# Kernel tuning notes

Hardware: AMD Instinct MI355X
Metric: run time of the kernel (lower is better)

The kernel has to match this reference:

```python
import jax, jax.numpy as jnp
import numpy as np

T, E, H, V, K = 1024, 300, 512, 100000, 12
START, STOP = 10, 11


def setup_inputs() -> dict:
    key = jax.random.key(0)
    ks = jax.random.split(key, 12)
    s = 0.05
    sentence = jax.random.randint(ks[0], (T,), 0, V, dtype=jnp.int32)
    tags = jax.random.randint(ks[1], (T,), 0, START, dtype=jnp.int32)  # real tags only
    word_embeds = jax.random.normal(ks[2], (V, E), jnp.float32) * 0.1

    def lstm_p(k):
        k1, k2 = jax.random.split(k)
        return (jax.random.normal(k1, (4 * H, E), jnp.float32) * s,
                jax.random.normal(k2, (4 * H, H), jnp.float32) * s,
                jnp.zeros(4 * H, jnp.float32), jnp.zeros(4 * H, jnp.float32))

    Wih_f, Whh_f, bih_f, bhh_f = lstm_p(ks[3])
    Wih_b, Whh_b, bih_b, bhh_b = lstm_p(ks[4])
    D = 2 * H
    attn_W = jax.random.normal(ks[5], (D, D), jnp.float32) * s
    attn_b = jnp.zeros(D, jnp.float32)
    h2h1_W = jax.random.normal(ks[6], (D, 2 * D), jnp.float32) * s
    h2h1_b = jnp.zeros(D, jnp.float32)
    tag_W = jax.random.normal(ks[7], (K, D), jnp.float32) * s
    tag_b = jnp.zeros(K, jnp.float32)
    transitions = jax.random.normal(ks[8], (K, K), jnp.float32) * 0.01
    transitions = transitions.at[START, :].set(-10000.0).at[:, STOP].set(-10000.0)
    return dict(sentence=sentence, tags=tags, word_embeds=word_embeds,
                Wih_f=Wih_f, Whh_f=Whh_f, bih_f=bih_f, bhh_f=bhh_f,
                Wih_b=Wih_b, Whh_b=Whh_b, bih_b=bih_b, bhh_b=bhh_b,
                attn_W=attn_W, attn_b=attn_b, h2h1_W=h2h1_W, h2h1_b=h2h1_b,
                tag_W=tag_W, tag_b=tag_b, transitions=transitions)


def _lstm_pass(x, Wih, Whh, bih, bhh):
    # x: [T, E] -> hs: [T, H]   (PyTorch LSTM gate order i,f,g,o)
    xg = x @ Wih.T + bih  # [T, 4H] precomputed input contribution

    def step(carry, g_in):
        h, c = carry
        g = g_in + h @ Whh.T + bhh
        i, f, gg, o = jnp.split(g, 4)
        i = jax.nn.sigmoid(i); f = jax.nn.sigmoid(f)
        gg = jnp.tanh(gg); o = jax.nn.sigmoid(o)
        c = f * c + i * gg
        h = o * jnp.tanh(c)
        return (h, c), h

    init = (jnp.zeros(H, x.dtype), jnp.zeros(H, x.dtype))
    _, hs = jax.lax.scan(step, init, xg)
    return hs


def reference(sentence, tags, word_embeds, Wih_f, Whh_f, bih_f, bhh_f,
              Wih_b, Whh_b, bih_b, bhh_b, attn_W, attn_b,
              h2h1_W, h2h1_b, tag_W, tag_b, transitions):
    x = word_embeds[sentence]                       # [T, E]  (dropout is eval no-op)
    h_fwd = _lstm_pass(x, Wih_f, Whh_f, bih_f, bhh_f)
    h_bwd = _lstm_pass(x[::-1], Wih_b, Whh_b, bih_b, bhh_b)[::-1]
    enc = jnp.concatenate([h_fwd, h_bwd], axis=-1)  # [T, 2H]

    # Attn 'general': energy(t, i) = enc[t] . (W enc[i] + b); vectorized per-timestep loop
    proj = enc @ attn_W.T + attn_b                  # [T, 2H]
    scores = enc @ proj.T                           # [T, T]
    w = jax.nn.softmax(scores, axis=-1)
    ctx = w @ enc                                   # [T, 2H]

    h1 = jnp.tanh(jnp.concatenate([enc, ctx], axis=-1) @ h2h1_W.T + h2h1_b)  # [T, 2H]
    feats = h1 @ tag_W.T + tag_b                    # [T, K]

    # CRF forward algorithm (log partition); transitions[to, from]
    alpha0 = jnp.full((K,), -10000.0, feats.dtype).at[START].set(0.0)

    def crf_step(alpha, feat):
        a = jax.nn.logsumexp(alpha[None, :] + transitions, axis=1) + feat
        return a, None

    alpha, _ = jax.lax.scan(crf_step, alpha0, feats)
    logZ = jax.nn.logsumexp(alpha + transitions[STOP])

    # gold path score (_score_sentence)
    pad_start = jnp.concatenate([jnp.array([START], tags.dtype), tags])
    pad_stop = jnp.concatenate([tags, jnp.array([STOP], tags.dtype)])
    gold = transitions[pad_stop, pad_start].sum() + feats[jnp.arange(T), tags].sum()

    return logZ - gold  # CRF negative log-likelihood for this sentence
```

## Files before the change

kernel.cpp:

```cpp
#include <hip/hip_runtime.h>
#include <hip/hip_fp16.h>

#define T_LEN 1024
#define E_DIM 300
#define H_DIM 512
#define D_DIM 1024
#define K_TAGS 12
#define G4 2048

typedef __attribute__((ext_vector_type(8))) short short8x;
typedef __attribute__((ext_vector_type(4))) float f32x4;

static __device__ __forceinline__ float frcp(float x){ return __builtin_amdgcn_rcpf(x); }
static __device__ __forceinline__ float sigm(float x){ return frcp(1.f + __expf(-x)); }
static __device__ __forceinline__ float ftanh(float x){
  const float e = __expf(2.f * fabsf(x));
  const float t = 1.f - 2.f * frcp(e + 1.f);
  return copysignf(t, x);
}
static __device__ __forceinline__ unsigned short f2b(float f){
  unsigned u = __float_as_uint(f);
  return (unsigned short)((u + 0x7fffu + ((u >> 16) & 1u)) >> 16);
}
static __device__ __forceinline__ uint4 pack8(const float* s){
  uint4 o;
  o.x = (unsigned)f2b(s[0]) | ((unsigned)f2b(s[1]) << 16);
  o.y = (unsigned)f2b(s[2]) | ((unsigned)f2b(s[3]) << 16);
  o.z = (unsigned)f2b(s[4]) | ((unsigned)f2b(s[5]) << 16);
  o.w = (unsigned)f2b(s[6]) | ((unsigned)f2b(s[7]) << 16);
  return o;
}
static __device__ __forceinline__ uint4 pack8u(const unsigned short* s){
  uint4 o;
  o.x = (unsigned)s[0] | ((unsigned)s[1] << 16);
  o.y = (unsigned)s[2] | ((unsigned)s[3] << 16);
  o.z = (unsigned)s[4] | ((unsigned)s[5] << 16);
  o.w = (unsigned)s[6] | ((unsigned)s[7] << 16);
  return o;
}

__global__ __launch_bounds__(256) void k_pre(
    const int* __restrict__ sent, const float* __restrict__ we,
    unsigned short* __restrict__ xh,
    const float* __restrict__ Wf, unsigned short* __restrict__ Wfh,
    const float* __restrict__ Wb, unsigned short* __restrict__ Wbh,
    unsigned* __restrict__ hbuf, unsigned* __restrict__ rdy)
{
  const int i = blockIdx.x*256 + threadIdx.x;
  if (i < 2048) hbuf[i] = 0u;
  else if (i < 2080) rdy[i-2048] = 0u;
  for (int g = i; g < T_LEN*E_DIM; g += 600*256){
    int t = g / E_DIM, e = g - t*E_DIM;
    xh[g] = f2b(we[(size_t)sent[t]*E_DIM + e]);
  }
  if (i < 153600){
    const float4 v = *reinterpret_cast<const float4*>(Wf + (size_t)i*4);
    ushort2 a, b;
    a.x = f2b(v.x); a.y = f2b(v.y); b.x = f2b(v.z); b.y = f2b(v.w);
    *reinterpret_cast<ushort2*>(Wfh + (size_t)i*4)     = a;
    *reinterpret_cast<ushort2*>(Wfh + (size_t)i*4 + 2) = b;
    const float4 u = *reinterpret_cast<const float4*>(Wb + (size_t)i*4);
    ushort2 c, d;
    c.x = f2b(u.x); c.y = f2b(u.y); d.x = f2b(u.z); d.y = f2b(u.w);
    *reinterpret_cast<ushort2*>(Wbh + (size_t)i*4)     = c;
    *reinterpret_cast<ushort2*>(Wbh + (size_t)i*4 + 2) = d;
  }
}

__global__ __launch_bounds__(256, 1) void k_lstm_fused(
    const float* __restrict__ Whh_f, const float* __restrict__ Whh_b,
    const float* __restrict__ bih_f, const float* __restrict__ bhh_f,
    const float* __restrict__ bih_b, const float* __restrict__ bhh_b,
    float* __restrict__ xg_f, float* __restrict__ xg_b,
    const unsigned short* __restrict__ xh,
    const unsigned short* __restrict__ Wih_fh, const unsigned short* __restrict__ Wih_bh,
    unsigned* __restrict__ hbuf, unsigned* __restrict__ xgReady,
    float* __restrict__ enc)
{
  __shared__ __align__(16) unsigned short As[64*40];
  __shared__ __align__(16) unsigned short Bs[64*40];
  __shared__ __align__(16) unsigned short lds_hb[512];
  __shared__ __align__(16) float raw[64];

  const int tid = threadIdx.x;
  const int wave = tid >> 6, lane = tid & 63;
  const int col = lane & 15, quad = lane >> 4;

  if (blockIdx.x >= 64){
    const int pid = blockIdx.x - 64;
    const int r  = tid >> 2, c8 = (tid & 3) * 8;
    const int wm = (wave >> 1) * 32, wn = (wave & 1) * 32;
    uint4* aw = (uint4*)(As + r*40 + c8);
    uint4* bw = (uint4*)(Bs + r*40 + c8);

    for (int j = pid; j < 1024; j += 192){
      const int bm = j >> 6, rem = j & 63, pdir = rem >> 5, bn = rem & 31;
      const unsigned short* Bh = pdir ? Wih_bh : Wih_fh;
      float* C = pdir ? xg_b : xg_f;
      const int am = pdir ? (1023 - (bm*64 + r)) : (bm*64 + r);
      const unsigned short* arow = xh + (size_t)am*E_DIM;
      const unsigned short* brow = Bh + (size_t)(bn*64 + r)*E_DIM;

      f32x4 acc[2][2];
      #pragma unroll
      for (int i=0;i<2;i++)
        #pragma unroll
        for (int jj=0;jj<2;jj++) acc[i][jj] = (f32x4){0.f,0.f,0.f,0.f};

      for (int k0 = 0; k0 < E_DIM; k0 += 32){
        uint4 avv, bvv;
        if (k0 + 32 <= E_DIM){
          avv = *(const uint4*)(arow + k0 + c8);
          bvv = *(const uint4*)(brow + k0 + c8);
        } else {
          unsigned short ta[8], tb[8];
          #pragma unroll
          for (int i=0;i<8;i++){
            const int kk = k0 + c8 + i;
            ta[i] = (kk < E_DIM) ? arow[kk] : (unsigned short)0;
            tb[i] = (kk < E_DIM) ? brow[kk] : (unsigned short)0;
          }
          avv = pack8u(ta); bvv = pack8u(tb);
        }
        __syncthreads();
        *aw = avv; *bw = bvv;
        __syncthreads();
        const short8x a0 = *(const short8x*)(As + (wm+col)*40    + quad*8);
        const short8x a1 = *(const short8x*)(As + (wm+16+col)*40 + quad*8);
        const short8x b0 = *(const short8x*)(Bs + (wn+col)*40    + quad*8);
        const short8x b1 = *(const short8x*)(Bs + (wn+16+col)*40 + quad*8);
        acc[0][0] = __builtin_amdgcn_mfma_f32_16x16x32_bf16(a0, b0, acc[0][0], 0, 0, 0);
        acc[0][1] = __builtin_amdgcn_mfma_f32_16x16x32_bf16(a0, b1, acc[0][1], 0, 0, 0);
        acc[1][0] = __builtin_amdgcn_mfma_f32_16x16x32_bf16(a1, b0, acc[1][0], 0, 0, 0);
        acc[1][1] = __builtin_amdgcn_mfma_f32_16x16x32_bf16(a1, b1, acc[1][1], 0, 0, 0);
      }
      #pragma unroll
      for (int mt=0;mt<2;mt++)
        #pragma unroll
        for (int nt=0;nt<2;nt++)
          #pragma unroll
          for (int i=0;i<4;i++)
            C[(size_t)(bm*64 + wm + 16*mt + quad*4 + i)*G4 + (bn*64 + wn + 16*nt + col)]
              = acc[mt][nt][i];
      __syncthreads();
      if (tid == 0)
        __hip_atomic_fetch_add(&xgReady[pdir*16 + bm], 1u,
                               __ATOMIC_RELEASE, __HIP_MEMORY_SCOPE_AGENT);
    }
    return;
  }

  const int dir = blockIdx.x >> 5;
  const int w   = blockIdx.x & 31;

  const float* Whh = dir ? Whh_b : Whh_f;
  const float* xg  = dir ? xg_b  : xg_f;
  unsigned* rdy = xgReady + dir*16;

  const int rowA = wave*H_DIM + w*16 + col;
  short8x w_frag[16];
  #pragma unroll
  for (int s=0;s<16;s++){
    const float* bp = Whh + (size_t)rowA*H_DIM + s*32 + quad*8;
    uint4 u = pack8(bp);
    w_frag[s] = *reinterpret_cast<short8x*>(&u);
  }

  float bias_r = 0.f, xg_cur = 0.f, c_reg = 0.f;
  int row2 = 0, readyBlk = 0;
  if (tid < 64){
    row2 = (tid >> 4)*H_DIM + w*16 + (tid & 15);
    bias_r = dir ? (bih_b[row2] + bhh_b[row2]) : (bih_f[row2] + bhh_f[row2]);
    while (__hip_atomic_load(rdy, __ATOMIC_RELAXED, __HIP_MEMORY_SCOPE_AGENT) != 32u) {}
    (void)__hip_atomic_load(rdy, __ATOMIC_ACQUIRE, __HIP_MEMORY_SCOPE_AGENT);
    readyBlk = 1;
    xg_cur = xg[row2];
  }

  unsigned* hb = hbuf + dir*1024;

  for (int t = 1; t <= T_LEN; ++t){
    {
      unsigned* s0 = hb + ((t-1)&1)*512 + tid;
      const unsigned want = (unsigned)(t-1);
      unsigned v0 = __hip_atomic_load(s0,     __ATOMIC_RELAXED, __HIP_MEMORY_SCOPE_AGENT);
      unsigned v1 = __hip_atomic_load(s0+256, __ATOMIC_RELAXED, __HIP_MEMORY_SCOPE_AGENT);
      while (((v0 >> 16) != want) || ((v1 >> 16) != want)){
        v0 = __hip_atomic_load(s0,     __ATOMIC_RELAXED, __HIP_MEMORY_SCOPE_AGENT);
        v1 = __hip_atomic_load(s0+256, __ATOMIC_RELAXED, __HIP_MEMORY_SCOPE_AGENT);
      }
      lds_hb[tid]     = (unsigned short)(v0 & 0xffffu);
      lds_hb[tid+256] = (unsigned short)(v1 & 0xffffu);
    }
    __syncthreads();

    float xg_nxt = 0.f;
    if (tid < 64 && t < T_LEN){
      const int nb = t >> 6;
      if (nb >= readyBlk){
        while (__hip_atomic_load(rdy + nb, __ATOMIC_RELAXED, __HIP_MEMORY_SCOPE_AGENT) != 32u) {}
        (void)__hip_atomic_load(rdy + nb, __ATOMIC_ACQUIRE, __HIP_MEMORY_SCOPE_AGENT);
        readyBlk = nb + 1;
      }
      xg_nxt = xg[(size_t)t*G4 + row2];
    }

    f32x4 a0 = (f32x4){0.f,0.f,0.f,0.f}, a1 = (f32x4){0.f,0.f,0.f,0.f};
    #pragma unroll
    for (int s=0;s<16;s+=2){
      const short8x b0 = *(const short8x*)(lds_hb + s*32     + quad*8);
      const short8x b1 = *(const short8x*)(lds_hb + (s+1)*32 + quad*8);
      a0 = __builtin_amdgcn_mfma_f32_16x16x32_bf16(w_frag[s],   b0, a0, 0, 0, 0);
      a1 = __builtin_amdgcn_mfma_f32_16x16x32_bf16(w_frag[s+1], b1, a1, 0, 0, 0);
    }
    if (col == 0){
      f32x4 asum = a0 + a1;
      *reinterpret_cast<f32x4*>(raw + wave*16 + quad*4) = asum;
    }
    __syncthreads();

    if (tid < 64){
      float v = raw[tid] + bias_r + xg_cur;
      const float va = ((tid >> 4) == 2) ? ftanh(v) : sigm(v);
      const int l2 = tid & 15;
      const float iv = __shfl(va, l2);
      const float fv = __shfl(va, l2 + 16);
      const float gg = __shfl(va, l2 + 32);
      const float ov = __shfl(va, l2 + 48);
      if (tid < 16){
        c_reg = fv*c_reg + iv*gg;
        const float hh = ov*ftanh(c_reg);
        const int hj = w*16 + tid;
        const unsigned hv = ((unsigned)t << 16) | (unsigned)f2b(hh);
        __hip_atomic_store(hb + (t&1)*512 + hj, hv,
                           __ATOMIC_RELAXED, __HIP_MEMORY_SCOPE_AGENT);
        const int tt = dir ? (T_LEN - t) : (t - 1);
        enc[(size_t)tt*D_DIM + dir*H_DIM + hj] = hh;
      }
      xg_cur = xg_nxt;
    }
    __syncthreads();
  }

  if (blockIdx.x == 0 && tid < 16)
    __hip_atomic_store(hbuf + tid, 0u, __ATOMIC_RELAXED, __HIP_MEMORY_SCOPE_AGENT);
}

static __device__ __forceinline__ void gbar(unsigned* c){
  __syncthreads();
  if (threadIdx.x == 0){
    __hip_atomic_fetch_add(c, 1u, __ATOMIC_RELEASE, __HIP_MEMORY_SCOPE_AGENT);
    while (__hip_atomic_load(c, __ATOMIC_RELAXED, __HIP_MEMORY_SCOPE_AGENT) != 256u) {}
    (void)__hip_atomic_load(c, __ATOMIC_ACQUIRE, __HIP_MEMORY_SCOPE_AGENT);
  }
  __syncthreads();
}

static __device__ void gemm_tile(
    const unsigned short* __restrict__ Ah, int lda,
    const unsigned short* __restrict__ Bh, int ldb,
    const float* __restrict__ bias, int act,
    void* __restrict__ Cp, int ldc, int cbf16, int K, int bm, int bn,
    unsigned short* As, unsigned short* Bs)
{
  const int tid = threadIdx.x;
  const int r  = tid >> 2, c8 = (tid & 3) * 8;
  const int wave = tid >> 6, lane = tid & 63;
  const int wm = (wave >> 1) * 32, wn = (wave & 1) * 32;
  const int col = lane & 15, quad = lane >> 4;

  const unsigned short* arow = Ah + (size_t)(bm+r)*lda;
  const unsigned short* brow = Bh + (size_t)(bn+r)*ldb;
  uint4* aw = (uint4*)(As + r*40 + c8);
  uint4* bw = (uint4*)(Bs + r*40 + c8);

  f32x4 acc[2][2];
  #pragma unroll
  for (int i=0;i<2;i++)
    #pragma unroll
    for (int j=0;j<2;j++) acc[i][j] = (f32x4){0.f,0.f,0.f,0.f};

  for (int k0 = 0; k0 < K; k0 += 32){
    const uint4 avv = *(const uint4*)(arow + k0 + c8);
    const uint4 bvv = *(const uint4*)(brow + k0 + c8);
    __syncthreads();
    *aw = avv; *bw = bvv;
    __syncthreads();
    const short8x a0 = *(const short8x*)(As + (wm+col)*40    + quad*8);
    const short8x a1 = *(const short8x*)(As + (wm+16+col)*40 + quad*8);
    const short8x b0 = *(const short8x*)(Bs + (wn+col)*40    + quad*8);
    const short8x b1 = *(const short8x*)(Bs + (wn+16+col)*40 + quad*8);
    acc[0][0] = __builtin_amdgcn_mfma_f32_16x16x32_bf16(a0, b0, acc[0][0], 0, 0, 0);
    acc[0][1] = __builtin_amdgcn_mfma_f32_16x16x32_bf16(a0, b1, acc[0][1], 0, 0, 0);
    acc[1][0] = __builtin_amdgcn_mfma_f32_16x16x32_bf16(a1, b0, acc[1][0], 0, 0, 0);
    acc[1][1] = __builtin_amdgcn_mfma_f32_16x16x32_bf16(a1, b1, acc[1][1], 0, 0, 0);
  }

  #pragma unroll
  for (int mt=0;mt<2;mt++){
    #pragma unroll
    for (int nt=0;nt<2;nt++){
      const int cc = bn + wn + 16*nt + col;
      const float bs = bias ? bias[cc] : 0.f;
      #pragma unroll
      for (int i=0;i<4;i++){
        const int rr = bm + wm + 16*mt + quad*4 + i;
        float v = acc[mt][nt][i] + bs;
        if (act) v = ftanh(v);
        if (cbf16) ((unsigned short*)Cp)[(size_t)rr*ldc + cc] = f2b(v);
        else       ((float*)Cp)[(size_t)rr*ldc + cc] = v;
      }
    }
  }
}

__global__ __launch_bounds__(256, 1) void k_tail(
    const float* __restrict__ enc,
    unsigned short* __restrict__ cath, unsigned short* __restrict__ encT,
    const float* __restrict__ attn_W, unsigned short* __restrict__ attn_Wh,
    const float* __restrict__ attn_b,
    const float* __restrict__ h2h1_W, unsigned short* __restrict__ h2h1_Wh,
    const float* __restrict__ h2h1_b,
    unsigned short* __restrict__ projh, float* __restrict__ scores,
    unsigned short* __restrict__ scoresh, float* __restrict__ h1,
    const float* __restrict__ tagW, const float* __restrict__ tagb,
    float* __restrict__ feats, const float* __restrict__ trans,
    const int* __restrict__ tags, float* __restrict__ chunkM,
    unsigned* __restrict__ bars, float* __restrict__ out)
{
  __shared__ __align__(16) unsigned short As[64*40];
  __shared__ __align__(16) unsigned short Bs[64*40];
  __shared__ float red[4], red2[4];
  const int tid = threadIdx.x, b = blockIdx.x;
  const int wave = tid >> 6, lane = tid & 63;
  const int bm = (b >> 4) * 64, bn = (b & 15) * 64;

  {
    float (*tile)[33] = (float(*)[33])As;
    const int tx = tid & 31, ty8 = tid >> 5;
    for (int j = b; j < 1024; j += 256){
      const int bx = (j & 31)*32, by = (j >> 5)*32;
      __syncthreads();
      #pragma unroll
      for (int i=ty8;i<32;i+=8){
        const float v = enc[(size_t)(by+i)*1024 + bx+tx];
        tile[i][tx] = v;
        cath[(size_t)(by+i)*2048 + bx+tx] = f2b(v);
      }
      __syncthreads();
      #pragma unroll
      for (int i=ty8;i<32;i+=8) encT[(size_t)(bx+i)*1024 + by+tx] = f2b(tile[tx][i]);
    }
    const int gid = b*256 + tid;
    for (int c = gid; c < 262144; c += 65536){
      const float4 v = *reinterpret_cast<const float4*>(attn_W + (size_t)c*4);
      ushort2 x, y; x.x=f2b(v.x); x.y=f2b(v.y); y.x=f2b(v.z); y.y=f2b(v.w);
      *reinterpret_cast<ushort2*>(attn_Wh + (size_t)c*4)     = x;
      *reinterpret_cast<ushort2*>(attn_Wh + (size_t)c*4 + 2) = y;
    }
    for (int c = gid; c < 524288; c += 65536){
      const float4 v = *reinterpret_cast<const float4*>(h2h1_W + (size_t)c*4);
      ushort2 x, y; x.x=f2b(v.x); x.y=f2b(v.y); y.x=f2b(v.z); y.y=f2b(v.w);
      *reinterpret_cast<ushort2*>(h2h1_Wh + (size_t)c*4)     = x;
      *reinterpret_cast<ushort2*>(h2h1_Wh + (size_t)c*4 + 2) = y;
    }
  }
  gbar(bars + 0);

  gemm_tile(cath, 2048, attn_Wh, D_DIM, attn_b, 0, projh, D_DIM, 1, D_DIM, bm, bn, As, Bs);
  gbar(bars + 1);

  gemm_tile(cath, 2048, projh, D_DIM, nullptr, 0, scores, T_LEN, 0, D_DIM, bm, bn, As, Bs);
  gbar(bars + 2);

  for (int rr = 0; rr < 4; ++rr){
    float* r = scores + (size_t)(b*4 + rr)*1024;
    unsigned short* rh = scoresh + (size_t)(b*4 + rr)*1024;
    float v[4];
    #pragma unroll
    for (int i=0;i<4;i++) v[i] = r[tid + i*256];
    float m = fmaxf(fmaxf(v[0],v[1]), fmaxf(v[2],v[3]));
    #pragma unroll
    for (int off=32; off>=1; off>>=1) m = fmaxf(m, __shfl_xor(m, off));
    if (lane == 0) red[wave] = m;
    __syncthreads();
    m = fmaxf(fmaxf(red[0],red[1]), fmaxf(red[2],red[3]));
    float s = 0.f;
    #pragma unroll
    for (int i=0;i<4;i++){ v[i] = __expf(v[i]-m); s += v[i]; }
    #pragma unroll
    for (int off=32; off>=1; off>>=1) s += __shfl_xor(s, off);
    if (lane == 0) red2[wave] = s;
    __syncthreads();
    s = red2[0]+red2[1]+red2[2]+red2[3];
    const float inv = frcp(s);
    #pragma unroll
    for (int i=0;i<4;i++){
      const float o = v[i]*inv;
      r[tid + i*256]  = o;
      rh[tid + i*256] = f2b(o);
    }
    __syncthreads();
  }
  gbar(bars + 3);

  gemm_tile(scoresh, T_LEN, encT, D_DIM, nullptr, 0, cath + 1024, 2048, 1, T_LEN, bm, bn, As, Bs);
  gbar(bars + 4);

  gemm_tile(cath, 2048, h2h1_Wh, 2048, h2h1_b, 1, h1, D_DIM, 0, 2048, bm, bn, As, Bs);
  gbar(bars + 5);

  for (int j = 0; j < 4; ++j){
    const int t = b*4 + j;
    const float* hr = h1 + (size_t)t*D_DIM;
    float hv[16];
    #pragma unroll
    for (int i=0;i<16;i++) hv[i] = hr[lane + 64*i];
    #pragma unroll
    for (int jj=0;jj<3;jj++){
      const int tag = wave*3 + jj;
      const float* wr = tagW + (size_t)tag*D_DIM;
      float s = 0.f;
      #pragma unroll
      for (int i=0;i<16;i++) s += hv[i]*wr[lane + 64*i];
      #pragma unroll
      for (int off=32; off>=1; off>>=1) s += __shfl_xor(s, off);
      if (lane == 0) feats[(size_t)t*K_TAGS + tag] = s + tagb[tag];
    }
  }
  gbar(bars + 6);

  if (b < 64){
    float* sT = (float*)Bs;
    float* sF = sT + 144;
    for (int q = tid; q < 144; q += 256) sT[q] = trans[q];
    const int t0 = b*16;
    for (int q = tid; q < 192; q += 256) sF[q] = feats[(size_t)t0*K_TAGS + q];
    __syncthreads();
    if (tid < 12){
      const int r = tid;
      float m[12], nm[12];
      #pragma unroll
      for (int k=0;k<12;k++) m[k] = sT[k*12 + r] + sF[k];
      for (int s=1; s<16; ++s){
        #pragma unroll
        for (int i=0;i<12;i++){
          float v[12]; float mx = -1e30f;
          #pragma unroll
          for (int k=0;k<12;k++){ v[k] = sT[i*12+k] + m[k]; mx = fmaxf(mx, v[k]); }
          float ss = 0.f;
          #pragma unroll
          for (int k=0;k<12;k++) ss += __expf(v[k]-mx);
          nm[i] = sF[s*12+i] + mx + __logf(ss);
        }
        #pragma unroll
        for (int i=0;i<12;i++) m[i] = nm[i];
      }
      #pragma unroll
      for (int k=0;k<12;k++) chunkM[b*144 + k*12 + r] = m[k];
    }
  }
  gbar(bars + 7);

  if (b == 0){
    float alpha = (lane == 10) ? 0.f : -10000.f;
    if (wave == 1){
      float g = 0.f;
      for (int i = lane; i <= T_LEN; i += 64){
        const int to = (i < T_LEN) ? tags[i]   : 11;
        const int fr = (i == 0)    ? 10        : tags[i-1];
        g += trans[to*K_TAGS + fr];
        if (i < T_LEN) g += feats[(size_t)i*K_TAGS + tags[i]];
      }
      #pragma unroll
      for (int off=32; off>=1; off>>=1) g += __shfl_xor(g, off);
      if (lane == 0) red[0] = g;
    } else if (wave == 0){
      float pf[12];
      #pragma unroll
      for (int k=0;k<12;k++) pf[k] = (lane < 12) ? chunkM[lane*12 + k] : 0.f;
      for (int c=0; c<64; ++c){
        float av[12];
        #pragma unroll
        for (int j=0;j<12;j++) av[j] = __shfl(alpha, j);
        float cur[12];
        #pragma unroll
        for (int k=0;k<12;k++) cur[k] = pf[k];
        if (c+1 < 64){
          #pragma unroll
          for (int k=0;k<12;k++)
            pf[k] = (lane < 12) ? chunkM[(c+1)*144 + lane*12 + k] : 0.f;
        }
        if (lane < 12){
          float v[12]; float mx = -1e30f;
          #pragma unroll
          for (int k=0;k<12;k++){ v[k] = cur[k] + av[k]; mx = fmaxf(mx, v[k]); }
          float ss = 0.f;
          #pragma unroll
          for (int k=0;k<12;k++) ss += __expf(v[k]-mx);
          alpha = mx + __logf(ss);
        }
      }
    }
    __syncthreads();
    if (wave == 0){
      float v = (lane < K_TAGS) ? (alpha + trans[11*K_TAGS + lane]) : -1e30f;
      float m = v;
      #pragma unroll
      for (int off=32; off>=1; off>>=1) m = fmaxf(m, __shfl_xor(m, off));
      float e = (lane < K_TAGS) ? __expf(v - m) : 0.f;
      #pragma unroll
      for (int off=32; off>=1; off>>=1) e += __shfl_xor(e, off);
      if (lane == 0) out[0] = (m + __logf(e)) - red[0];
    }
  }
}

extern "C" void kernel_launch(void* const* d_in, const int* in_sizes, int n_in,
                              void* d_out, int out_size, void* d_ws, size_t ws_size,
                              hipStream_t stream)
{
  const int*   sentence = (const int*)d_in[0];
  const int*   tags     = (const int*)d_in[1];
  const float* we       = (const float*)d_in[2];
  const float* Wih_f    = (const float*)d_in[3];
  const float* Whh_f    = (const float*)d_in[4];
  const float* bih_f    = (const float*)d_in[5];
  const float* bhh_f    = (const float*)d_in[6];
  const float* Wih_b    = (const float*)d_in[7];
  const float* Whh_b    = (const float*)d_in[8];
  const float* bih_b    = (const float*)d_in[9];
  const float* bhh_b    = (const float*)d_in[10];
  const float* attn_W   = (const float*)d_in[11];
  const float* attn_b   = (const float*)d_in[12];
  const float* h2h1_W   = (const float*)d_in[13];
  const float* h2h1_b   = (const float*)d_in[14];
  const float* tag_W    = (const float*)d_in[15];
  const float* tag_b    = (const float*)d_in[16];
  const float* trans    = (const float*)d_in[17];
  float* out = (float*)d_out;

  float* ws = (float*)d_ws;
  float* R1 = ws;
  float* R2 = ws + 2097152;
  float* R3 = ws + 4194304;
  float* R4 = ws + 5242880;
  float* feats = ws + 6291456;
  unsigned* hbuf = (unsigned*)(ws + 6303744);

  float* xg_f = R1;
  float* xg_b = R2;
  float* enc  = R3;
  unsigned short* xh      = (unsigned short*)R4;
  unsigned short* Wih_fh  = (unsigned short*)R4 + 307200;
  unsigned short* Wih_bh  = (unsigned short*)R4 + 921600;
  unsigned* xgReady = (unsigned*)feats;
  unsigned short* cath    = (unsigned short*)R1;
  unsigned short* attn_Wh = (unsigned short*)(R1 + 1048576);
  unsigned short* h2h1_Wh = (unsigned short*)R2;
  float* scores = R2 + 1048576;
  unsigned short* encT    = (unsigned short*)R4;
  unsigned short* projh   = (unsigned short*)R4 + 1048576;
  unsigned short* scoresh = (unsigned short*)R3;
  float* h1     = R3;
  float* chunkM = R4;

  k_pre<<<dim3(600), dim3(256), 0, stream>>>(sentence, we, xh,
      Wih_f, Wih_fh, Wih_b, Wih_bh, hbuf, xgReady);
  k_lstm_fused<<<dim3(256), dim3(256), 0, stream>>>(Whh_f, Whh_b, bih_f, bhh_f,
      bih_b, bhh_b, xg_f, xg_b, xh, Wih_fh, Wih_bh, hbuf, xgReady, enc);
  k_tail<<<dim3(256), dim3(256), 0, stream>>>(enc, cath, encT,
      attn_W, attn_Wh, attn_b, h2h1_W, h2h1_Wh, h2h1_b,
      projh, scores, scoresh, h1, tag_W, tag_b, feats, trans, tags,
      chunkM, hbuf, out);
}
```

Before: 1.906 ms.

## Use 128x128 GEMM tiles on 64 blocks and flag-array grid barrier

The tail kernel's four dense GEMMs move from 64x64 tiles spread over 256 blocks to 128x128 tiles computed by the first 64 blocks. Each wave now issues a 4x4 grid of MFMAs per k-step, which raises operand reuse from shared memory. The grid barrier changes from one atomic counter to per-block phase flags, padded 16 words apart. Each thread polls one block's flag, so the single-address contention goes away. The cost is that 192 blocks sit idle during the GEMMs, plus more accumulator registers and twice the LDS per block.

```diff
diff --git a/kernel.cpp b/kernel.cpp
--- a/kernel.cpp
+++ b/kernel.cpp
@@ -75,7 +75,7 @@
     const unsigned short* __restrict__ xh,
     const unsigned short* __restrict__ Wih_fh, const unsigned short* __restrict__ Wih_bh,
     unsigned* __restrict__ hbuf, unsigned* __restrict__ xgReady,
-    float* __restrict__ enc)
+    unsigned* __restrict__ flags, float* __restrict__ enc)
 {
   __shared__ __align__(16) unsigned short As[64*40];
   __shared__ __align__(16) unsigned short Bs[64*40];
@@ -242,21 +242,23 @@
     __syncthreads();
   }
 
-  if (blockIdx.x == 0 && tid < 16)
-    __hip_atomic_store(hbuf + tid, 0u, __ATOMIC_RELAXED, __HIP_MEMORY_SCOPE_AGENT);
-}
-
-static __device__ __forceinline__ void gbar(unsigned* c){
+  if (blockIdx.x == 0)
+    for (int i = tid; i < 4096; i += 256)
+      __hip_atomic_store(flags + i, 0u, __ATOMIC_RELAXED, __HIP_MEMORY_SCOPE_AGENT);
+}
+
+static __device__ __forceinline__ void gbar(unsigned* flags, unsigned phase){
   __syncthreads();
-  if (threadIdx.x == 0){
-    __hip_atomic_fetch_add(c, 1u, __ATOMIC_RELEASE, __HIP_MEMORY_SCOPE_AGENT);
-    while (__hip_atomic_load(c, __ATOMIC_RELAXED, __HIP_MEMORY_SCOPE_AGENT) != 256u) {}
-    (void)__hip_atomic_load(c, __ATOMIC_ACQUIRE, __HIP_MEMORY_SCOPE_AGENT);
-  }
+  if (threadIdx.x == 0)
+    __hip_atomic_store(flags + blockIdx.x*16, phase,
+                       __ATOMIC_RELEASE, __HIP_MEMORY_SCOPE_AGENT);
+  unsigned* myw = flags + threadIdx.x*16;
+  while (__hip_atomic_load(myw, __ATOMIC_RELAXED, __HIP_MEMORY_SCOPE_AGENT) < phase) {}
+  (void)__hip_atomic_load(myw, __ATOMIC_ACQUIRE, __HIP_MEMORY_SCOPE_AGENT);
   __syncthreads();
 }
 
-static __device__ void gemm_tile(
+static __device__ void gemm128(
     const unsigned short* __restrict__ Ah, int lda,
     const unsigned short* __restrict__ Bh, int ldb,
     const float* __restrict__ bias, int act,
@@ -264,42 +266,47 @@
     unsigned short* As, unsigned short* Bs)
 {
   const int tid = threadIdx.x;
-  const int r  = tid >> 2, c8 = (tid & 3) * 8;
+  const int r = tid >> 1, c16 = (tid & 1) * 16;
   const int wave = tid >> 6, lane = tid & 63;
-  const int wm = (wave >> 1) * 32, wn = (wave & 1) * 32;
+  const int wm = (wave >> 1) * 64, wn = (wave & 1) * 64;
   const int col = lane & 15, quad = lane >> 4;
 
-  const unsigned short* arow = Ah + (size_t)(bm+r)*lda;
-  const unsigned short* brow = Bh + (size_t)(bn+r)*ldb;
-  uint4* aw = (uint4*)(As + r*40 + c8);
-  uint4* bw = (uint4*)(Bs + r*40 + c8);
-
-  f32x4 acc[2][2];
+  const unsigned short* arow = Ah + (size_t)(bm + r)*lda + c16;
+  const unsigned short* brow = Bh + (size_t)(bn + r)*ldb + c16;
+  uint4* aw = (uint4*)(As + r*40 + c16);
+  uint4* bw = (uint4*)(Bs + r*40 + c16);
+
+  f32x4 acc[4][4];
   #pragma unroll
-  for (int i=0;i<2;i++)
-    #pragma unroll
-    for (int j=0;j<2;j++) acc[i][j] = (f32x4){0.f,0.f,0.f,0.f};
+  for (int i=0;i<4;i++)
+    #pragma unroll
+    for (int j=0;j<4;j++) acc[i][j] = (f32x4){0.f,0.f,0.f,0.f};
 
   for (int k0 = 0; k0 < K; k0 += 32){
-    const uint4 avv = *(const uint4*)(arow + k0 + c8);
-    const uint4 bvv = *(const uint4*)(brow + k0 + c8);
-    __syncthreads();
-    *aw = avv; *bw = bvv;
-    __syncthreads();
-    const short8x a0 = *(const short8x*)(As + (wm+col)*40    + quad*8);
-    const short8x a1 = *(const short8x*)(As + (wm+16+col)*40 + quad*8);
-    const short8x b0 = *(const short8x*)(Bs + (wn+col)*40    + quad*8);
-    const short8x b1 = *(const short8x*)(Bs + (wn+16+col)*40 + quad*8);
-    acc[0][0] = __builtin_amdgcn_mfma_f32_16x16x32_bf16(a0, b0, acc[0][0], 0, 0, 0);
-    acc[0][1] = __builtin_amdgcn_mfma_f32_16x16x32_bf16(a0, b1, acc[0][1], 0, 0, 0);
-    acc[1][0] = __builtin_amdgcn_mfma_f32_16x16x32_bf16(a1, b0, acc[1][0], 0, 0, 0);
-    acc[1][1] = __builtin_amdgcn_mfma_f32_16x16x32_bf16(a1, b1, acc[1][1], 0, 0, 0);
+    const uint4 a0v = *(const uint4*)(arow + k0);
+    const uint4 a1v = *(const uint4*)(arow + k0 + 8);
+    const uint4 b0v = *(const uint4*)(brow + k0);
+    const uint4 b1v = *(const uint4*)(brow + k0 + 8);
+    __syncthreads();
+    aw[0] = a0v; aw[1] = a1v;
+    bw[0] = b0v; bw[1] = b1v;
+    __syncthreads();
+    short8x af[4], bf[4];
+    #pragma unroll
+    for (int m=0;m<4;m++) af[m] = *(const short8x*)(As + (wm + m*16 + col)*40 + quad*8);
+    #pragma unroll
+    for (int n=0;n<4;n++) bf[n] = *(const short8x*)(Bs + (wn + n*16 + col)*40 + quad*8);
+    #pragma unroll
+    for (int m=0;m<4;m++)
+      #pragma unroll
+      for (int n=0;n<4;n++)
+        acc[m][n] = __builtin_amdgcn_mfma_f32_16x16x32_bf16(af[m], bf[n], acc[m][n], 0, 0, 0);
   }
 
   #pragma unroll
-  for (int mt=0;mt<2;mt++){
-    #pragma unroll
-    for (int nt=0;nt<2;nt++){
+  for (int mt=0;mt<4;mt++){
+    #pragma unroll
+    for (int nt=0;nt<4;nt++){
       const int cc = bn + wn + 16*nt + col;
       const float bs = bias ? bias[cc] : 0.f;
       #pragma unroll
@@ -326,14 +333,14 @@
     const float* __restrict__ tagW, const float* __restrict__ tagb,
     float* __restrict__ feats, const float* __restrict__ trans,
     const int* __restrict__ tags, float* __restrict__ chunkM,
-    unsigned* __restrict__ bars, float* __restrict__ out)
+    unsigned* __restrict__ flags, float* __restrict__ out)
 {
-  __shared__ __align__(16) unsigned short As[64*40];
-  __shared__ __align__(16) unsigned short Bs[64*40];
+  __shared__ __align__(16) unsigned short As[128*40];
+  __shared__ __align__(16) unsigned short Bs[128*40];
   __shared__ float red[4], red2[4];
   const int tid = threadIdx.x, b = blockIdx.x;
   const int wave = tid >> 6, lane = tid & 63;
-  const int bm = (b >> 4) * 64, bn = (b & 15) * 64;
+  const int bm = (b >> 3) * 128, bn = (b & 7) * 128;
 
   {
     float (*tile)[33] = (float(*)[33])As;
@@ -365,13 +372,13 @@
       *reinterpret_cast<ushort2*>(h2h1_Wh + (size_t)c*4 + 2) = y;
     }
   }
-  gbar(bars + 0);
-
-  gemm_tile(cath, 2048, attn_Wh, D_DIM, attn_b, 0, projh, D_DIM, 1, D_DIM, bm, bn, As, Bs);
-  gbar(bars + 1);
-
-  gemm_tile(cath, 2048, projh, D_DIM, nullptr, 0, scores, T_LEN, 0, D_DIM, bm, bn, As, Bs);
-  gbar(bars + 2);
+  gbar(flags, 1);
+
+  if (b < 64) gemm128(cath, 2048, attn_Wh, D_DIM, attn_b, 0, projh, D_DIM, 1, D_DIM, bm, bn, As, Bs);
+  gbar(flags, 2);
+
+  if (b < 64) gemm128(cath, 2048, projh, D_DIM, nullptr, 0, scores, T_LEN, 0, D_DIM, bm, bn, As, Bs);
+  gbar(flags, 3);
 
   for (int rr = 0; rr < 4; ++rr){
     float* r = scores + (size_t)(b*4 + rr)*1024;
@@ -402,13 +409,13 @@
     }
     __syncthreads();
   }
-  gbar(bars + 3);
-
-  gemm_tile(scoresh, T_LEN, encT, D_DIM, nullptr, 0, cath + 1024, 2048, 1, T_LEN, bm, bn, As, Bs);
-  gbar(bars + 4);
-
-  gemm_tile(cath, 2048, h2h1_Wh, 2048, h2h1_b, 1, h1, D_DIM, 0, 2048, bm, bn, As, Bs);
-  gbar(bars + 5);
+  gbar(flags, 4);
+
+  if (b < 64) gemm128(scoresh, T_LEN, encT, D_DIM, nullptr, 0, cath + 1024, 2048, 1, T_LEN, bm, bn, As, Bs);
+  gbar(flags, 5);
+
+  if (b < 64) gemm128(cath, 2048, h2h1_Wh, 2048, h2h1_b, 1, h1, D_DIM, 0, 2048, bm, bn, As, Bs);
+  gbar(flags, 6);
 
   for (int j = 0; j < 4; ++j){
     const int t = b*4 + j;
@@ -428,7 +435,7 @@
       if (lane == 0) feats[(size_t)t*K_TAGS + tag] = s + tagb[tag];
     }
   }
-  gbar(bars + 6);
+  gbar(flags, 7);
 
   if (b < 64){
     float* sT = (float*)Bs;
@@ -460,7 +467,7 @@
       for (int k=0;k<12;k++) chunkM[b*144 + k*12 + r] = m[k];
     }
   }
-  gbar(bars + 7);
+  gbar(flags, 8);
 
   if (b == 0){
     float alpha = (lane == 10) ? 0.f : -10000.f;
@@ -557,6 +564,7 @@
   unsigned* xgReady = (unsigned*)feats;
   unsigned short* cath    = (unsigned short*)R1;
   unsigned short* attn_Wh = (unsigned short*)(R1 + 1048576);
+  unsigned* flags = (unsigned*)(R1 + 1572864);
   unsigned short* h2h1_Wh = (unsigned short*)R2;
   float* scores = R2 + 1048576;
   unsigned short* encT    = (unsigned short*)R4;
@@ -568,9 +576,9 @@
   k_pre<<<dim3(600), dim3(256), 0, stream>>>(sentence, we, xh,
       Wih_f, Wih_fh, Wih_b, Wih_bh, hbuf, xgReady);
   k_lstm_fused<<<dim3(256), dim3(256), 0, stream>>>(Whh_f, Whh_b, bih_f, bhh_f,
-      bih_b, bhh_b, xg_f, xg_b, xh, Wih_fh, Wih_bh, hbuf, xgReady, enc);
+      bih_b, bhh_b, xg_f, xg_b, xh, Wih_fh, Wih_bh, hbuf, xgReady, flags, enc);
   k_tail<<<dim3(256), dim3(256), 0, stream>>>(enc, cath, encT,
       attn_W, attn_Wh, attn_b, h2h1_W, h2h1_Wh, h2h1_b,
       projh, scores, scoresh, h1, tag_W, tag_b, feats, trans, tags,
-      chunkM, hbuf, out);
-}
+      chunkM, flags, out);
+}
```

Result: slower. 1.956 ms (+2.6%).

## Remap LSTM gate rows per wave to drop LDS exchange; use flag-array grid barrier

Applied to the files above, without the earlier changes.

The recurrent Whh rows are permuted so each wave's MFMA output holds all four gates for four hidden units. Gate activations and the cell update then run inside each wave with shuffles, which removes the LDS staging buffer and one __syncthreads per timestep on the serial LSTM critical path. The tail kernel's counter-based grid barrier is replaced by per-block phase flags polled by all threads, so blocks no longer contend on a single atomic; the LSTM kernel clears the flags at the end. This adds more polling traffic and relies on the flags being reset correctly between calls.

```diff
diff --git a/kernel.cpp b/kernel.cpp
--- a/kernel.cpp
+++ b/kernel.cpp
@@ -75,12 +75,11 @@
     const unsigned short* __restrict__ xh,
     const unsigned short* __restrict__ Wih_fh, const unsigned short* __restrict__ Wih_bh,
     unsigned* __restrict__ hbuf, unsigned* __restrict__ xgReady,
-    float* __restrict__ enc)
+    unsigned* __restrict__ flags, float* __restrict__ enc)
 {
   __shared__ __align__(16) unsigned short As[64*40];
   __shared__ __align__(16) unsigned short Bs[64*40];
   __shared__ __align__(16) unsigned short lds_hb[512];
-  __shared__ __align__(16) float raw[64];
 
   const int tid = threadIdx.x;
   const int wave = tid >> 6, lane = tid & 63;
@@ -157,7 +156,7 @@
   const float* xg  = dir ? xg_b  : xg_f;
   unsigned* rdy = xgReady + dir*16;
 
-  const int rowA = wave*H_DIM + w*16 + col;
+  const int rowA = (col >> 2)*H_DIM + w*16 + wave*4 + (col & 3);
   short8x w_frag[16];
   #pragma unroll
   for (int s=0;s<16;s++){
@@ -166,16 +165,20 @@
     w_frag[s] = *reinterpret_cast<short8x*>(&u);
   }
 
-  float bias_r = 0.f, xg_cur = 0.f, c_reg = 0.f;
-  int row2 = 0, readyBlk = 0;
-  if (tid < 64){
-    row2 = (tid >> 4)*H_DIM + w*16 + (tid & 15);
-    bias_r = dir ? (bih_b[row2] + bhh_b[row2]) : (bih_f[row2] + bhh_f[row2]);
+  const bool act_ln = (col == 0);
+  const int gbase = quad*H_DIM + w*16 + wave*4;
+  f32x4 bias4 = (f32x4){0.f,0.f,0.f,0.f}, xg4 = (f32x4){0.f,0.f,0.f,0.f};
+  int readyBlk = 1;
+  if (act_ln){
+    const float4 b1 = *reinterpret_cast<const float4*>((dir?bih_b:bih_f) + gbase);
+    const float4 b2 = *reinterpret_cast<const float4*>((dir?bhh_b:bhh_f) + gbase);
+    bias4[0]=b1.x+b2.x; bias4[1]=b1.y+b2.y; bias4[2]=b1.z+b2.z; bias4[3]=b1.w+b2.w;
     while (__hip_atomic_load(rdy, __ATOMIC_RELAXED, __HIP_MEMORY_SCOPE_AGENT) != 32u) {}
     (void)__hip_atomic_load(rdy, __ATOMIC_ACQUIRE, __HIP_MEMORY_SCOPE_AGENT);
-    readyBlk = 1;
-    xg_cur = xg[row2];
-  }
+    const float4 x0 = *reinterpret_cast<const float4*>(xg + gbase);
+    xg4[0]=x0.x; xg4[1]=x0.y; xg4[2]=x0.z; xg4[3]=x0.w;
+  }
+  float c_reg = 0.f;
 
   unsigned* hb = hbuf + dir*1024;
 
@@ -194,15 +197,16 @@
     }
     __syncthreads();
 
-    float xg_nxt = 0.f;
-    if (tid < 64 && t < T_LEN){
+    f32x4 xg_nxt = (f32x4){0.f,0.f,0.f,0.f};
+    if (act_ln && t < T_LEN){
       const int nb = t >> 6;
       if (nb >= readyBlk){
         while (__hip_atomic_load(rdy + nb, __ATOMIC_RELAXED, __HIP_MEMORY_SCOPE_AGENT) != 32u) {}
         (void)__hip_atomic_load(rdy + nb, __ATOMIC_ACQUIRE, __HIP_MEMORY_SCOPE_AGENT);
         readyBlk = nb + 1;
       }
-      xg_nxt = xg[(size_t)t*G4 + row2];
+      const float4 xx = *reinterpret_cast<const float4*>(xg + (size_t)t*G4 + gbase);
+      xg_nxt[0]=xx.x; xg_nxt[1]=xx.y; xg_nxt[2]=xx.z; xg_nxt[3]=xx.w;
     }
 
     f32x4 a0 = (f32x4){0.f,0.f,0.f,0.f}, a1 = (f32x4){0.f,0.f,0.f,0.f};
@@ -213,46 +217,55 @@
       a0 = __builtin_amdgcn_mfma_f32_16x16x32_bf16(w_frag[s],   b0, a0, 0, 0, 0);
       a1 = __builtin_amdgcn_mfma_f32_16x16x32_bf16(w_frag[s+1], b1, a1, 0, 0, 0);
     }
-    if (col == 0){
-      f32x4 asum = a0 + a1;
-      *reinterpret_cast<f32x4*>(raw + wave*16 + quad*4) = asum;
-    }
-    __syncthreads();
-
-    if (tid < 64){
-      float v = raw[tid] + bias_r + xg_cur;
-      const float va = ((tid >> 4) == 2) ? ftanh(v) : sigm(v);
-      const int l2 = tid & 15;
-      const float iv = __shfl(va, l2);
-      const float fv = __shfl(va, l2 + 16);
-      const float gg = __shfl(va, l2 + 32);
-      const float ov = __shfl(va, l2 + 48);
-      if (tid < 16){
-        c_reg = fv*c_reg + iv*gg;
-        const float hh = ov*ftanh(c_reg);
-        const int hj = w*16 + tid;
-        const unsigned hv = ((unsigned)t << 16) | (unsigned)f2b(hh);
-        __hip_atomic_store(hb + (t&1)*512 + hj, hv,
-                           __ATOMIC_RELAXED, __HIP_MEMORY_SCOPE_AGENT);
-        const int tt = dir ? (T_LEN - t) : (t - 1);
-        enc[(size_t)tt*D_DIM + dir*H_DIM + hj] = hh;
-      }
-      xg_cur = xg_nxt;
-    }
-    __syncthreads();
-  }
-
-  if (blockIdx.x == 0 && tid < 16)
-    __hip_atomic_store(hbuf + tid, 0u, __ATOMIC_RELAXED, __HIP_MEMORY_SCOPE_AGENT);
-}
-
-static __device__ __forceinline__ void gbar(unsigned* c){
+
+    f32x4 va = (f32x4){0.f,0.f,0.f,0.f};
+    {
+      const f32x4 asum = a0 + a1;
+      if (act_ln){
+        #pragma unroll
+        for (int j=0;j<4;j++){
+          const float v = asum[j] + bias4[j] + xg4[j];
+          va[j] = (quad == 2) ? ftanh(v) : sigm(v);
+        }
+      }
+    }
+    float h_val = 0.f;
+    #pragma unroll
+    for (int du=0; du<4; ++du){
+      const float iv = __shfl(va[du], 0);
+      const float fv = __shfl(va[du], 16);
+      const float gv = __shfl(va[du], 32);
+      const float ov = __shfl(va[du], 48);
+      if (lane == du){
+        c_reg = fv*c_reg + iv*gv;
+        h_val = ov*ftanh(c_reg);
+      }
+    }
+    if (lane < 4){
+      const int hj = w*16 + wave*4 + lane;
+      const unsigned hv = ((unsigned)t << 16) | (unsigned)f2b(h_val);
+      __hip_atomic_store(hb + (t&1)*512 + hj, hv,
+                         __ATOMIC_RELAXED, __HIP_MEMORY_SCOPE_AGENT);
+      const int tt = dir ? (T_LEN - t) : (t - 1);
+      enc[(size_t)tt*D_DIM + dir*H_DIM + hj] = h_val;
+    }
+    if (act_ln) xg4 = xg_nxt;
+    __syncthreads();
+  }
+
+  if (blockIdx.x == 0)
+    for (int i = tid; i < 4096; i += 256)
+      __hip_atomic_store(flags + i, 0u, __ATOMIC_RELAXED, __HIP_MEMORY_SCOPE_AGENT);
+}
+
+static __device__ __forceinline__ void gbar(unsigned* flags, unsigned phase){
   __syncthreads();
-  if (threadIdx.x == 0){
-    __hip_atomic_fetch_add(c, 1u, __ATOMIC_RELEASE, __HIP_MEMORY_SCOPE_AGENT);
-    while (__hip_atomic_load(c, __ATOMIC_RELAXED, __HIP_MEMORY_SCOPE_AGENT) != 256u) {}
-    (void)__hip_atomic_load(c, __ATOMIC_ACQUIRE, __HIP_MEMORY_SCOPE_AGENT);
-  }
+  if (threadIdx.x == 0)
+    __hip_atomic_store(flags + blockIdx.x*16, phase,
+                       __ATOMIC_RELEASE, __HIP_MEMORY_SCOPE_AGENT);
+  unsigned* myw = flags + threadIdx.x*16;
+  while (__hip_atomic_load(myw, __ATOMIC_RELAXED, __HIP_MEMORY_SCOPE_AGENT) < phase) {}
+  (void)__hip_atomic_load(myw, __ATOMIC_ACQUIRE, __HIP_MEMORY_SCOPE_AGENT);
   __syncthreads();
 }
 
@@ -326,7 +339,7 @@
     const float* __restrict__ tagW, const float* __restrict__ tagb,
     float* __restrict__ feats, const float* __restrict__ trans,
     const int* __restrict__ tags, float* __restrict__ chunkM,
-    unsigned* __restrict__ bars, float* __restrict__ out)
+    unsigned* __restrict__ flags, float* __restrict__ out)
 {
   __shared__ __align__(16) unsigned short As[64*40];
   __shared__ __align__(16) unsigned short Bs[64*40];
@@ -365,13 +378,13 @@
       *reinterpret_cast<ushort2*>(h2h1_Wh + (size_t)c*4 + 2) = y;
     }
   }
-  gbar(bars + 0);
+  gbar(flags, 1);
 
   gemm_tile(cath, 2048, attn_Wh, D_DIM, attn_b, 0, projh, D_DIM, 1, D_DIM, bm, bn, As, Bs);
-  gbar(bars + 1);
+  gbar(flags, 2);
 
   gemm_tile(cath, 2048, projh, D_DIM, nullptr, 0, scores, T_LEN, 0, D_DIM, bm, bn, As, Bs);
-  gbar(bars + 2);
+  gbar(flags, 3);
 
   for (int rr = 0; rr < 4; ++rr){
     float* r = scores + (size_t)(b*4 + rr)*1024;
@@ -402,13 +415,13 @@
     }
     __syncthreads();
   }
-  gbar(bars + 3);
+  gbar(flags, 4);
 
   gemm_tile(scoresh, T_LEN, encT, D_DIM, nullptr, 0, cath + 1024, 2048, 1, T_LEN, bm, bn, As, Bs);
-  gbar(bars + 4);
+  gbar(flags, 5);
 
   gemm_tile(cath, 2048, h2h1_Wh, 2048, h2h1_b, 1, h1, D_DIM, 0, 2048, bm, bn, As, Bs);
-  gbar(bars + 5);
+  gbar(flags, 6);
 
   for (int j = 0; j < 4; ++j){
     const int t = b*4 + j;
@@ -428,7 +441,7 @@
       if (lane == 0) feats[(size_t)t*K_TAGS + tag] = s + tagb[tag];
     }
   }
-  gbar(bars + 6);
+  gbar(flags, 7);
 
   if (b < 64){
     float* sT = (float*)Bs;
@@ -460,7 +473,7 @@
       for (int k=0;k<12;k++) chunkM[b*144 + k*12 + r] = m[k];
     }
   }
-  gbar(bars + 7);
+  gbar(flags, 8);
 
   if (b == 0){
     float alpha = (lane == 10) ? 0.f : -10000.f;
@@ -557,6 +570,7 @@
   unsigned* xgReady = (unsigned*)feats;
   unsigned short* cath    = (unsigned short*)R1;
   unsigned short* attn_Wh = (unsigned short*)(R1 + 1048576);
+  unsigned* flags = (unsigned*)(R1 + 1572864);
   unsigned short* h2h1_Wh = (unsigned short*)R2;
   float* scores = R2 + 1048576;
   unsigned short* encT    = (unsigned short*)R4;
@@ -568,9 +582,9 @@
   k_pre<<<dim3(600), dim3(256), 0, stream>>>(sentence, we, xh,
       Wih_f, Wih_fh, Wih_b, Wih_bh, hbuf, xgReady);
   k_lstm_fused<<<dim3(256), dim3(256), 0, stream>>>(Whh_f, Whh_b, bih_f, bhh_f,
-      bih_b, bhh_b, xg_f, xg_b, xh, Wih_fh, Wih_bh, hbuf, xgReady, enc);
+      bih_b, bhh_b, xg_f, xg_b, xh, Wih_fh, Wih_bh, hbuf, xgReady, flags, enc);
   k_tail<<<dim3(256), dim3(256), 0, stream>>>(enc, cath, encT,
       attn_W, attn_Wh, attn_b, h2h1_W, h2h1_Wh, h2h1_b,
       projh, scores, scoresh, h1, tag_W, tag_b, feats, trans, tags,
-      chunkM, hbuf, out);
-}
+      chunkM, flags, out);
+}
```

Result: slower. 2.349 ms (+23.3%).
